# Kernel tuning notes

Hardware: AMD Instinct MI355X
Metric: run time of the kernel (lower is better)

Reference implementation:

```python
import jax, jax.numpy as jnp
import numpy as np

N_EMBD = 1024
N_HEAD = 16
BLOCK_SIZE = 2048
HEAD_DIM = N_EMBD // N_HEAD
NEG_INF = -1e10


def precompute_rotary_emb(dim, max_positions):
    positions = jnp.arange(max_positions, dtype=jnp.float32)
    freqs = 1.0 / 10000.0 ** (jnp.arange(0, dim, 2, dtype=jnp.float32) / dim)
    t_theta = jnp.outer(positions, freqs)  # (max_positions, dim//2)
    return jnp.stack([jnp.cos(t_theta), jnp.sin(t_theta)], axis=-1)  # (P, dim//2, 2)


def setup_inputs() -> dict:
    key = jax.random.key(0)
    ks = jax.random.split(key, 9)
    s = 1.0 / np.sqrt(N_EMBD)
    x = jax.random.normal(ks[0], (2, 2048, N_EMBD), dtype=jnp.float32)
    Wq = jax.random.uniform(ks[1], (N_EMBD, N_EMBD), minval=-s, maxval=s)
    bq = jax.random.uniform(ks[2], (N_EMBD,), minval=-s, maxval=s)
    Wk = jax.random.uniform(ks[3], (N_EMBD, N_EMBD), minval=-s, maxval=s)
    bk = jax.random.uniform(ks[4], (N_EMBD,), minval=-s, maxval=s)
    Wv = jax.random.uniform(ks[5], (N_EMBD, N_EMBD), minval=-s, maxval=s)
    bv = jax.random.uniform(ks[6], (N_EMBD,), minval=-s, maxval=s)
    Wp = jax.random.uniform(ks[7], (N_EMBD, N_EMBD), minval=-s, maxval=s)
    bp = jax.random.uniform(ks[8], (N_EMBD,), minval=-s, maxval=s)
    rope_cache = precompute_rotary_emb(HEAD_DIM, BLOCK_SIZE)
    return {"x": x, "Wq": Wq, "bq": bq, "Wk": Wk, "bk": bk,
            "Wv": Wv, "bv": bv, "Wp": Wp, "bp": bp, "rope_cache": rope_cache}


def _apply_rope(t, rope_cache, T):
    # t: (B, T, H, hd); rope applied per-head, vectorized over H
    B, _, H, hd = t.shape
    cos = rope_cache[:T, :, 0][None, :, None, :]  # (1, T, 1, hd//2)
    sin = rope_cache[:T, :, 1][None, :, None, :]
    tr = t.reshape(B, T, H, hd // 2, 2)
    real = tr[..., 0] * cos - tr[..., 1] * sin
    imag = tr[..., 0] * sin + tr[..., 1] * cos
    return jnp.stack([real, imag], axis=-1).reshape(B, T, H, hd)


def reference(x, Wq, bq, Wk, bk, Wv, bv, Wp, bp, rope_cache):
    B, T, C = x.shape
    H, hd = N_HEAD, C // N_HEAD
    q = (x @ Wq.T + bq).reshape(B, T, H, hd)
    k = (x @ Wk.T + bk).reshape(B, T, H, hd)
    v = (x @ Wv.T + bv).reshape(B, T, H, hd)
    q = _apply_rope(q, rope_cache, T)
    k = _apply_rope(k, rope_cache, T)
    # (B, H, T, T)
    att = jnp.einsum('bthd,bshd->bhts', q, k) / jnp.sqrt(jnp.float32(hd))
    causal = jnp.tril(jnp.ones((T, T), dtype=bool))
    att = jnp.where(causal[None, None], att, NEG_INF)
    att = jax.nn.softmax(att, axis=-1)
    y = jnp.einsum('bhts,bshd->bthd', att, v).reshape(B, T, C)
    return y @ Wp.T + bp
```

## Files before the change

kernel.cpp:

```cpp
#include <hip/hip_runtime.h>
#include <hip/hip_bf16.h>
#include <stdint.h>

#define N_EMBD 1024
#define T_SEQ  2048
#define NB     2
#define NH     16
#define HD     64
#define BTROWS (NB*T_SEQ)

typedef __attribute__((ext_vector_type(8))) short s16x8;
typedef __attribute__((ext_vector_type(4))) short s16x4;
typedef __attribute__((ext_vector_type(4))) float f32x4;

__device__ __forceinline__ unsigned short f2bf(float f) {
    union { float f; unsigned int u; } c; c.f = f;
    unsigned int u = c.u;
    unsigned int r = (u + 0x7fffu + ((u >> 16) & 1u)) >> 16;
    return (unsigned short)r;
}

__device__ __forceinline__ unsigned int pack2bf(float a, float b) {
    __hip_bfloat162 h = __float22bfloat162_rn(make_float2(a, b));
    union { __hip_bfloat162 h; unsigned int u; } c; c.h = h;
    return c.u;
}

#define GLDS16(gsrc, ldst) \
  __builtin_amdgcn_global_load_lds((const __attribute__((address_space(1))) unsigned int*)(gsrc), \
                                   (__attribute__((address_space(3))) unsigned int*)(ldst), 16, 0, 0)

__global__ void cast_all(const float* __restrict__ x,  const float* __restrict__ wq,
                         const float* __restrict__ wk, const float* __restrict__ wv,
                         const float* __restrict__ wp, unsigned short* __restrict__ dst) {
    const int i = blockIdx.x * 256 + threadIdx.x;
    const float* src; int off;
    if (i < 1048576) { src = x; off = i; }
    else {
        const int j = i - 1048576;
        const int w = j >> 18;
        off = j & 262143;
        src = (w == 0) ? wq : (w == 1) ? wk : (w == 2) ? wv : wp;
    }
    float4 v = reinterpret_cast<const float4*>(src)[off];
    ushort4 o;
    o.x = f2bf(v.x); o.y = f2bf(v.y); o.z = f2bf(v.z); o.w = f2bf(v.w);
    reinterpret_cast<ushort4*>(dst)[i] = o;
}

__global__ __launch_bounds__(256)
void gemm_qkv(const unsigned short* __restrict__ A,
              const unsigned short* __restrict__ Wb,
              const float* __restrict__ bq, const float* __restrict__ bk, const float* __restrict__ bv,
              unsigned short* __restrict__ Ob,
              const float* __restrict__ rope)
{
    constexpr int K = 1024, N = 1024;
    const int z = blockIdx.z;
    const unsigned short* Bt = Wb + (size_t)z * 1048576;
    const float* bias = (z == 0) ? bq : (z == 1) ? bk : bv;
    unsigned short* outp = Ob + (size_t)z * 4194304;
    const bool dorope = (z < 2);

    __shared__ unsigned short Al[128*32];
    __shared__ unsigned short Bl[128*32];
    const int tid = threadIdx.x;
    const int w = tid >> 6, l = tid & 63;
    const int bm = blockIdx.x * 128;
    const int bn = blockIdx.y * 128;
    const int wr = (w >> 1) * 64, wc = (w & 1) * 64;
    const int lr = l & 15, lg = l >> 4;
    const int scol = (l & 3) * 8;
    const int srow_in = l >> 2;

    f32x4 acc[4][4] = {};

    for (int k0 = 0; k0 < K; k0 += 32) {
        #pragma unroll
        for (int j = 0; j < 2; ++j) {
            const int i = w*2 + j;
            const int row = i*16 + srow_in;
            GLDS16(A  + (size_t)(bm+row)*K + k0 + scol, Al + i*512);
            GLDS16(Bt + (size_t)(bn+row)*K + k0 + scol, Bl + i*512);
        }
        __syncthreads();
        s16x8 af[4], bfv[4];
        #pragma unroll
        for (int m = 0; m < 4; ++m)
            af[m] = *(const s16x8*)(Al + (wr + m*16 + lr)*32 + lg*8);
        #pragma unroll
        for (int n = 0; n < 4; ++n)
            bfv[n] = *(const s16x8*)(Bl + (wc + n*16 + lr)*32 + lg*8);
        #pragma unroll
        for (int m = 0; m < 4; ++m)
            #pragma unroll
            for (int n = 0; n < 4; ++n)
                acc[m][n] = __builtin_amdgcn_mfma_f32_16x16x32_bf16(af[m], bfv[n], acc[m][n], 0, 0, 0);
        __syncthreads();
    }

    #pragma unroll
    for (int m = 0; m < 4; ++m) {
        const int row0 = bm + wr + m*16 + lg*4;
        #pragma unroll
        for (int n = 0; n < 4; ++n) {
            const int colg = bn + wc + n*16 + lr;
            const float bb = bias[colg];
            if (z == 2) {
                const int h = colg >> 6, d2 = colg & (HD-1);
                const int b_ = row0 >> 11, t0 = row0 & (T_SEQ-1);
                ushort4 st;
                st.x = f2bf(acc[m][n][0] + bb);
                st.y = f2bf(acc[m][n][1] + bb);
                st.z = f2bf(acc[m][n][2] + bb);
                st.w = f2bf(acc[m][n][3] + bb);
                *(ushort4*)(outp + ((size_t)(b_*NH + h)*HD + d2)*T_SEQ + t0) = st;
            } else {
                #pragma unroll
                for (int r = 0; r < 4; ++r) {
                    const float val = acc[m][n][r] + bb;
                    const int bt = row0 + r;
                    const float pairv = __shfl_xor(val, 1);
                    const int t = bt & (T_SEQ-1);
                    const int d = colg & (HD-1);
                    const float2 cs = *(const float2*)(rope + (size_t)t*HD + (d >> 1)*2);
                    const float res = (d & 1) ? fmaf(pairv, cs.y,  val*cs.x)
                                              : fmaf(-pairv, cs.y, val*cs.x);
                    const int b_ = bt >> 11, h = colg >> 6, d2 = colg & (HD-1);
                    outp[(((size_t)(b_*NH + h))*T_SEQ + t)*HD + d2] = f2bf(res);
                }
            }
        }
    }
}

__global__ __launch_bounds__(256)
void gemm_proj(const unsigned short* __restrict__ A,
               const unsigned short* __restrict__ Bt,
               const float* __restrict__ bias,
               float* __restrict__ outp)
{
    constexpr int K = 1024, N = 1024;
    __shared__ unsigned short Al[128*32];
    __shared__ unsigned short Bl[128*32];
    const int tid = threadIdx.x;
    const int w = tid >> 6, l = tid & 63;
    const int bm = blockIdx.x * 128;
    const int bn = blockIdx.y * 128;
    const int wr = (w >> 1) * 64, wc = (w & 1) * 64;
    const int lr = l & 15, lg = l >> 4;
    const int scol = (l & 3) * 8;
    const int srow_in = l >> 2;

    f32x4 acc[4][4] = {};

    for (int k0 = 0; k0 < K; k0 += 32) {
        #pragma unroll
        for (int j = 0; j < 2; ++j) {
            const int i = w*2 + j;
            const int row = i*16 + srow_in;
            GLDS16(A  + (size_t)(bm+row)*K + k0 + scol, Al + i*512);
            GLDS16(Bt + (size_t)(bn+row)*K + k0 + scol, Bl + i*512);
        }
        __syncthreads();
        s16x8 af[4], bfv[4];
        #pragma unroll
        for (int m = 0; m < 4; ++m)
            af[m] = *(const s16x8*)(Al + (wr + m*16 + lr)*32 + lg*8);
        #pragma unroll
        for (int n = 0; n < 4; ++n)
            bfv[n] = *(const s16x8*)(Bl + (wc + n*16 + lr)*32 + lg*8);
        #pragma unroll
        for (int m = 0; m < 4; ++m)
            #pragma unroll
            for (int n = 0; n < 4; ++n)
                acc[m][n] = __builtin_amdgcn_mfma_f32_16x16x32_bf16(af[m], bfv[n], acc[m][n], 0, 0, 0);
        __syncthreads();
    }

    #pragma unroll
    for (int m = 0; m < 4; ++m) {
        const int row0 = bm + wr + m*16 + lg*4;
        #pragma unroll
        for (int n = 0; n < 4; ++n) {
            const int colg = bn + wc + n*16 + lr;
            const float bb = bias[colg];
            #pragma unroll
            for (int r = 0; r < 4; ++r)
                outp[(size_t)(row0 + r)*N + colg] = acc[m][n][r] + bb;
        }
    }
}

__global__ __launch_bounds__(256)
void flash4(const unsigned short* __restrict__ Qg, const unsigned short* __restrict__ Kg,
            const unsigned short* __restrict__ VTg, unsigned short* __restrict__ Y)
{
    __shared__ unsigned short Kl[2][4096];
    __shared__ unsigned short Vl[2][4096];

    const int tid = threadIdx.x, w = tid >> 6, l = tid & 63;
    const int lr = l & 15, lg = l >> 4;
    const int u = blockIdx.x >> 5, bh = blockIdx.x & 31;
    const int qb = (u < 16) ? (31 - u) : (u - 16);
    const int b_ = bh >> 4, hh = bh & (NH-1);

    const unsigned short* Qb = Qg  + (size_t)bh*T_SEQ*HD;
    const unsigned short* Kb = Kg  + (size_t)bh*T_SEQ*HD;
    const unsigned short* Vb = VTg + (size_t)bh*HD*T_SEQ;

    int soK[2], soV[2];
    #pragma unroll
    for (int i = 0; i < 2; ++i) {
        const int p = i*256 + tid;
        const int row = p >> 3, ps = p & 7;
        soK[i] = row*HD    + ((ps ^ (row & 7))*8);
        soV[i] = row*T_SEQ + ((ps ^ (row & 7))*8);
    }

    const int q0 = qb*64;
    const int nt = qb + 1;
    const int qrow = q0 + w*16 + lr;

    s16x8 qf[2];
    #pragma unroll
    for (int kk = 0; kk < 2; ++kk)
        qf[kk] = *(const s16x8*)(Qb + (size_t)qrow*HD + kk*32 + lg*8);

    f32x4 oacc[4] = {};
    float mrun = -3.0e38f, lrun = 0.0f;

    #pragma unroll
    for (int i = 0; i < 2; ++i) {
        GLDS16(Kb + soK[i], &Kl[0][(i*256 + w*64)*8]);
        GLDS16(Vb + soV[i], &Vl[0][(i*256 + w*64)*8]);
    }
    __syncthreads();

    int cur = 0;
    for (int t = 0; t < nt; ++t) {
        if (t + 1 < nt) {
            #pragma unroll
            for (int i = 0; i < 2; ++i) {
                GLDS16(Kb + (size_t)(t+1)*64*HD + soK[i], &Kl[cur^1][(i*256 + w*64)*8]);
                GLDS16(Vb + (size_t)(t+1)*64    + soV[i], &Vl[cur^1][(i*256 + w*64)*8]);
            }
        }

        f32x4 sac[4] = {};
        __builtin_amdgcn_s_setprio(1);
        #pragma unroll
        for (int kkd = 0; kkd < 2; ++kkd) {
            const int off = ((kkd*4 + lg) ^ (lr & 7)) * 8;
            #pragma unroll
            for (int n = 0; n < 4; ++n) {
                s16x8 kf = *(const s16x8*)&Kl[cur][(n*16 + lr)*64 + off];
                sac[n] = __builtin_amdgcn_mfma_f32_16x16x32_bf16(kf, qf[kkd], sac[n], 0, 0, 0);
            }
        }
        __builtin_amdgcn_s_setprio(0);

        float p[4][4];
        float pm = -3.0e38f;
        const bool maskt = (t == qb);
        #pragma unroll
        for (int n = 0; n < 4; ++n)
            #pragma unroll
            for (int r = 0; r < 4; ++r) {
                float s = sac[n][r] * 0.125f;
                if (maskt && (t*64 + n*16 + lg*4 + r > qrow)) s = -1e10f;
                p[n][r] = s;
                pm = fmaxf(pm, s);
            }
        pm = fmaxf(pm, __shfl_xor(pm, 16));
        pm = fmaxf(pm, __shfl_xor(pm, 32));
        const bool defer = __all(pm <= mrun + 8.0f) != 0;
        const float mnew = defer ? mrun : fmaxf(mrun, pm);
        float ls = 0.0f;
        #pragma unroll
        for (int n = 0; n < 4; ++n)
            #pragma unroll
            for (int r = 0; r < 4; ++r) {
                const float e = __expf(p[n][r] - mnew);
                p[n][r] = e;
                ls += e;
            }
        ls += __shfl_xor(ls, 16);
        ls += __shfl_xor(ls, 32);
        if (!defer) {
            const float corr = __expf(mrun - mnew);
            mrun = mnew;
            lrun = lrun * corr + ls;
            float corrv[4];
            #pragma unroll
            for (int r = 0; r < 4; ++r) corrv[r] = __shfl(corr, lg*4 + r);
            #pragma unroll
            for (int n = 0; n < 4; ++n)
                #pragma unroll
                for (int r = 0; r < 4; ++r) oacc[n][r] *= corrv[r];
        } else {
            lrun += ls;
        }

        __builtin_amdgcn_s_setprio(1);
        #pragma unroll
        for (int kk2 = 0; kk2 < 2; ++kk2) {
            union { s16x8 v; unsigned uu[4]; } pa;
            pa.uu[0] = pack2bf(p[2*kk2][0],   p[2*kk2][1]);
            pa.uu[1] = pack2bf(p[2*kk2][2],   p[2*kk2][3]);
            pa.uu[2] = pack2bf(p[2*kk2+1][0], p[2*kk2+1][1]);
            pa.uu[3] = pack2bf(p[2*kk2+1][2], p[2*kk2+1][3]);
            #pragma unroll
            for (int n = 0; n < 4; ++n) {
                const int d = n*16 + lr;
                const int c0 = (4*kk2     + (lg >> 1)) ^ (lr & 7);
                const int c1 = (4*kk2 + 2 + (lg >> 1)) ^ (lr & 7);
                union { s16x8 v; s16x4 q[2]; } vf;
                vf.q[0] = *(const s16x4*)&Vl[cur][d*64 + c0*8 + (lg & 1)*4];
                vf.q[1] = *(const s16x4*)&Vl[cur][d*64 + c1*8 + (lg & 1)*4];
                oacc[n] = __builtin_amdgcn_mfma_f32_16x16x32_bf16(pa.v, vf.v, oacc[n], 0, 0, 0);
            }
        }
        __builtin_amdgcn_s_setprio(0);

        __syncthreads();
        cur ^= 1;
    }

    const float linv = 1.0f / lrun;
    float invv[4];
    #pragma unroll
    for (int r = 0; r < 4; ++r) invv[r] = __shfl(linv, lg*4 + r);
    #pragma unroll
    for (int r = 0; r < 4; ++r) {
        const int tq = q0 + w*16 + lg*4 + r;
        const size_t base = ((size_t)(b_*T_SEQ + tq))*N_EMBD + hh*HD;
        #pragma unroll
        for (int n = 0; n < 4; ++n)
            Y[base + n*16 + lr] = f2bf(oacc[n][r] * invv[r]);
    }
}

#define MB(x) ((size_t)(x) << 20)

extern "C" void kernel_launch(void* const* d_in, const int* in_sizes, int n_in,
                              void* d_out, int out_size, void* d_ws, size_t ws_size,
                              hipStream_t stream) {
    const float* x    = (const float*)d_in[0];
    const float* Wq   = (const float*)d_in[1];
    const float* bq   = (const float*)d_in[2];
    const float* Wk   = (const float*)d_in[3];
    const float* bk   = (const float*)d_in[4];
    const float* Wv   = (const float*)d_in[5];
    const float* bv   = (const float*)d_in[6];
    const float* Wp   = (const float*)d_in[7];
    const float* bp   = (const float*)d_in[8];
    const float* rope = (const float*)d_in[9];

    char* ws = (char*)d_ws;
    unsigned short* xb  = (unsigned short*)(ws + MB(0));
    unsigned short* Wqb = (unsigned short*)(ws + MB(8));
    unsigned short* Wpb = (unsigned short*)(ws + MB(14));
    unsigned short* Qa  = (unsigned short*)(ws + MB(16));
    unsigned short* y2  = (unsigned short*)(ws + MB(40));

    cast_all<<<8192, 256, 0, stream>>>(x, Wq, Wk, Wv, Wp, xb);

    gemm_qkv<<<dim3(BTROWS/128, N_EMBD/128, 3), 256, 0, stream>>>(xb, Wqb, bq, bk, bv, Qa, rope);

    flash4<<<1024, 256, 0, stream>>>(Qa, Qa + 4194304, Qa + 8388608, y2);

    gemm_proj<<<dim3(BTROWS/128, N_EMBD/128), 256, 0, stream>>>(y2, Wpb, bp, (float*)d_out);
}
```

Baseline: 213.9 us.

## Double-buffer LDS tiles in QKV and projection GEMMs

Both GEMM kernels now use two LDS buffers and prefetch the next K-slice with global-to-LDS loads while MFMAs run on the current slice, leaving one barrier per iteration instead of two. The QKV launch folds the z dimension into blockIdx.y (a 24-wide y grid), which changes block ordering and may affect L2 reuse of the weights. The cost is double the LDS per block, which can reduce occupancy.

```diff
diff --git a/kernel.cpp b/kernel.cpp
--- a/kernel.cpp
+++ b/kernel.cpp
@@ -55,48 +55,54 @@
               unsigned short* __restrict__ Ob,
               const float* __restrict__ rope)
 {
-    constexpr int K = 1024, N = 1024;
-    const int z = blockIdx.z;
-    const unsigned short* Bt = Wb + (size_t)z * 1048576;
+    constexpr int K = 1024;
+    const int z  = blockIdx.y >> 3;
+    const int bn = (blockIdx.y & 7) * 128;
     const float* bias = (z == 0) ? bq : (z == 1) ? bk : bv;
     unsigned short* outp = Ob + (size_t)z * 4194304;
-    const bool dorope = (z < 2);
-
-    __shared__ unsigned short Al[128*32];
-    __shared__ unsigned short Bl[128*32];
+
+    __shared__ unsigned short Al[2][4096];
+    __shared__ unsigned short Bl[2][4096];
     const int tid = threadIdx.x;
     const int w = tid >> 6, l = tid & 63;
     const int bm = blockIdx.x * 128;
-    const int bn = blockIdx.y * 128;
     const int wr = (w >> 1) * 64, wc = (w & 1) * 64;
     const int lr = l & 15, lg = l >> 4;
     const int scol = (l & 3) * 8;
     const int srow_in = l >> 2;
+    const size_t brow0 = (size_t)(z*1024 + bn);
 
     f32x4 acc[4][4] = {};
 
-    for (int k0 = 0; k0 < K; k0 += 32) {
+    auto stage = [&](int k0, int buf) {
         #pragma unroll
         for (int j = 0; j < 2; ++j) {
             const int i = w*2 + j;
             const int row = i*16 + srow_in;
-            GLDS16(A  + (size_t)(bm+row)*K + k0 + scol, Al + i*512);
-            GLDS16(Bt + (size_t)(bn+row)*K + k0 + scol, Bl + i*512);
-        }
-        __syncthreads();
+            GLDS16(A  + (size_t)(bm+row)*K + k0 + scol, &Al[buf][i*512]);
+            GLDS16(Wb + (brow0+row)*K      + k0 + scol, &Bl[buf][i*512]);
+        }
+    };
+
+    stage(0, 0);
+    __syncthreads();
+    int cur = 0;
+    for (int t = 0; t < 32; ++t) {
+        if (t < 31) stage((t+1)*32, cur^1);
         s16x8 af[4], bfv[4];
         #pragma unroll
         for (int m = 0; m < 4; ++m)
-            af[m] = *(const s16x8*)(Al + (wr + m*16 + lr)*32 + lg*8);
-        #pragma unroll
-        for (int n = 0; n < 4; ++n)
-            bfv[n] = *(const s16x8*)(Bl + (wc + n*16 + lr)*32 + lg*8);
+            af[m] = *(const s16x8*)(&Al[cur][(wr + m*16 + lr)*32 + lg*8]);
+        #pragma unroll
+        for (int n = 0; n < 4; ++n)
+            bfv[n] = *(const s16x8*)(&Bl[cur][(wc + n*16 + lr)*32 + lg*8]);
         #pragma unroll
         for (int m = 0; m < 4; ++m)
             #pragma unroll
             for (int n = 0; n < 4; ++n)
                 acc[m][n] = __builtin_amdgcn_mfma_f32_16x16x32_bf16(af[m], bfv[n], acc[m][n], 0, 0, 0);
         __syncthreads();
+        cur ^= 1;
     }
 
     #pragma unroll
@@ -141,8 +147,8 @@
                float* __restrict__ outp)
 {
     constexpr int K = 1024, N = 1024;
-    __shared__ unsigned short Al[128*32];
-    __shared__ unsigned short Bl[128*32];
+    __shared__ unsigned short Al[2][4096];
+    __shared__ unsigned short Bl[2][4096];
     const int tid = threadIdx.x;
     const int w = tid >> 6, l = tid & 63;
     const int bm = blockIdx.x * 128;
@@ -154,28 +160,35 @@
 
     f32x4 acc[4][4] = {};
 
-    for (int k0 = 0; k0 < K; k0 += 32) {
+    auto stage = [&](int k0, int buf) {
         #pragma unroll
         for (int j = 0; j < 2; ++j) {
             const int i = w*2 + j;
             const int row = i*16 + srow_in;
-            GLDS16(A  + (size_t)(bm+row)*K + k0 + scol, Al + i*512);
-            GLDS16(Bt + (size_t)(bn+row)*K + k0 + scol, Bl + i*512);
-        }
-        __syncthreads();
+            GLDS16(A  + (size_t)(bm+row)*K + k0 + scol, &Al[buf][i*512]);
+            GLDS16(Bt + (size_t)(bn+row)*K + k0 + scol, &Bl[buf][i*512]);
+        }
+    };
+
+    stage(0, 0);
+    __syncthreads();
+    int cur = 0;
+    for (int t = 0; t < 32; ++t) {
+        if (t < 31) stage((t+1)*32, cur^1);
         s16x8 af[4], bfv[4];
         #pragma unroll
         for (int m = 0; m < 4; ++m)
-            af[m] = *(const s16x8*)(Al + (wr + m*16 + lr)*32 + lg*8);
-        #pragma unroll
-        for (int n = 0; n < 4; ++n)
-            bfv[n] = *(const s16x8*)(Bl + (wc + n*16 + lr)*32 + lg*8);
+            af[m] = *(const s16x8*)(&Al[cur][(wr + m*16 + lr)*32 + lg*8]);
+        #pragma unroll
+        for (int n = 0; n < 4; ++n)
+            bfv[n] = *(const s16x8*)(&Bl[cur][(wc + n*16 + lr)*32 + lg*8]);
         #pragma unroll
         for (int m = 0; m < 4; ++m)
             #pragma unroll
             for (int n = 0; n < 4; ++n)
                 acc[m][n] = __builtin_amdgcn_mfma_f32_16x16x32_bf16(af[m], bfv[n], acc[m][n], 0, 0, 0);
         __syncthreads();
+        cur ^= 1;
     }
 
     #pragma unroll
@@ -366,7 +379,7 @@
 
     cast_all<<<8192, 256, 0, stream>>>(x, Wq, Wk, Wv, Wp, xb);
 
-    gemm_qkv<<<dim3(BTROWS/128, N_EMBD/128, 3), 256, 0, stream>>>(xb, Wqb, bq, bk, bv, Qa, rope);
+    gemm_qkv<<<dim3(BTROWS/128, 24), 256, 0, stream>>>(xb, Wqb, bq, bk, bv, Qa, rope);
 
     flash4<<<1024, 256, 0, stream>>>(Qa, Qa + 4194304, Qa + 8388608, y2);
 
```

New measurement: 206.8 us. -3.3%, faster.
